# Performance work log

Measured on AMD Instinct MI355X. Metric: run time of the kernel, lower is better.

The kernel has to match this reference:

```python
import jax, jax.numpy as jnp
import numpy as np


def setup_inputs() -> dict:
    key = jax.random.key(0)
    ks = jax.random.split(key, 10)
    B, T, D = 256, 256, 256
    CH, L, K = 128, 3, 10          # chunk_size, levels, conv_size
    H = CH * L                     # hidden_dim = 384
    G = 4 * H + 2 * L              # gate projection width = 1542
    HS = H // 6

    def xavier(k, shape):
        fan_in, fan_out = shape[0], shape[-1]
        lim = np.sqrt(6.0 / (fan_in + fan_out)).astype(np.float32)
        return jax.random.uniform(k, shape, jnp.float32, -lim, lim)

    x = jax.random.normal(ks[0], (B, T, D), jnp.float32)
    lengths = jax.random.randint(ks[1], (B,), 1, T + 1).astype(jnp.int64)
    Wk = xavier(ks[2], (D + 1, G)); bk = jnp.zeros((G,), jnp.float32)
    Wr = xavier(ks[3], (H + 1, G)); br = jnp.zeros((G,), jnp.float32)
    Ws = xavier(ks[4], (H, HS));    bs = jnp.zeros((HS,), jnp.float32)
    Wrs = xavier(ks[5], (HS, H));   brs = jnp.zeros((H,), jnp.float32)
    Wc = xavier(ks[6], (H, H, K)) / np.sqrt(K)  # Conv1d weight (out, in, k)
    bc = jnp.zeros((H,), jnp.float32)
    return {"x": x, "lengths": lengths, "Wk": Wk, "bk": bk, "Wr": Wr,
            "br": br, "Ws": Ws, "bs": bs, "Wrs": Wrs, "brs": brs,
            "Wc": Wc, "bc": bc}


def _cumax_l2r(z):
    return jnp.cumsum(jax.nn.softmax(z, axis=-1), axis=-1)


def _cumax_r2l(z):
    zf = jnp.flip(z, -1)
    return jnp.flip(jnp.cumsum(jax.nn.softmax(zf, axis=-1), axis=-1), -1)


def reference(x, lengths, Wk, bk, Wr, br, Ws, bs, Wrs, brs, Wc, bc):
    B, T, D = x.shape
    H = Wr.shape[0] - 1
    G = Wk.shape[1]
    L = (G - 4 * H) // 2
    CH = H // L
    K = Wc.shape[2]
    ones = jnp.ones((B, 1), x.dtype)

    def step(carry, xt):
        c, h, tmp_h, tmp_dis = carry
        # two linear projections (interval == 1 always)
        xo = (jnp.concatenate([xt, ones], -1) @ Wk + bk
              + jnp.concatenate([h, ones], -1) @ Wr + br)
        fm = _cumax_l2r(xo[:, :L])[:, :, None]          # (B,L,1)
        im = _cumax_r2l(xo[:, L:2 * L])[:, :, None]     # (B,L,1)
        rest = xo[:, 2 * L:].reshape(B, 4 * L, CH)
        f = jax.nn.sigmoid(rest[:, :L])
        i = jax.nn.sigmoid(rest[:, L:2 * L])
        o = jax.nn.sigmoid(rest[:, 2 * L:3 * L])
        c_in = jnp.tanh(rest[:, 3 * L:])
        c_last = c.reshape(B, L, CH)
        ov = fm * im
        c_new = (ov * (f * c_last + i * c_in)
                 + (fm - ov) * c_last + (im - ov) * c_in)
        h_new = (o * jnp.tanh(c_new)).reshape(B, H)
        c_new = c_new.reshape(B, H)
        cur_dis = 1.0 - jnp.mean(fm[..., 0], axis=-1)   # (B,)
        # sliding buffers (K, B, H) and (K, B)
        tmp_h = jnp.concatenate([tmp_h[1:], h_new[None]], 0)
        tmp_dis = jnp.concatenate([tmp_dis[1:], cur_dis[None]], 0)
        # local window attention weights
        ld = jax.nn.softmax(jnp.cumsum(tmp_dis.T, axis=1), axis=1)  # (B,K)
        local_h = tmp_h.transpose(1, 2, 0) * ld[:, None, :]         # (B,H,K)
        theme = jax.nn.sigmoid(
            jax.nn.relu(jnp.mean(local_h, -1) @ Ws + bs) @ Wrs + brs)
        conv = jnp.einsum('bhk,ohk->bo', local_h, Wc) + bc          # valid conv -> len 1
        local_out = theme * conv
        return (c_new, h_new, tmp_h, tmp_dis), (h_new, local_out)

    c0 = jnp.zeros((B, H), x.dtype)
    h0 = jnp.zeros((B, H), x.dtype)
    th0 = jnp.zeros((K, B, H), x.dtype)
    td0 = jnp.zeros((K, B), x.dtype)
    _, (origin_h, loc_h) = jax.lax.scan(step, (c0, h0, th0, td0),
                                        x.transpose(1, 0, 2))
    output = (loc_h + origin_h).transpose(1, 0, 2)   # (B,T,H)
    idx = jnp.clip(lengths, 1, T).astype(jnp.int32) - 1
    last_output = output[jnp.arange(B), idx]
    return (last_output, output)
```

## Files before the change

### kernel.cpp

```cpp
#include <hip/hip_runtime.h>
#include <hip/hip_bf16.h>
#include <cstddef>

#define B_  256
#define T_  256
#define D_  256
#define H_  384
#define G_  1542
#define L_  3
#define CH_ 128
#define K_  10
#define HS_ 64

#define NGRP 16
#define NMEM 16
#define GW   16
#define CPM  24
#define NFR  7
#define PCOLS 112
#define XOLP 114
#define NKC  20
#define W_LDS    (NKC * NFR * 64 * 8 * 2)
#define BIAS_OFF W_LDS
#define UNI_OFF  (W_LDS + 512)
#define LDS_BYTES (UNI_OFF + 12288)

#define POST_LDS 107520

#define SENT 0xFFFFFFFFFFFFFFFFull

using bf16x8 = __attribute__((ext_vector_type(8))) short;
using f32x4  = __attribute__((ext_vector_type(4))) float;
typedef unsigned long long ull_t;

__device__ __forceinline__ float bf2f(unsigned short s) {
    return __uint_as_float(((unsigned)s) << 16);
}
__device__ __forceinline__ unsigned short f2bf(float f) {
    unsigned u = __float_as_uint(f);
    return (unsigned short)((u + 0x7fffu + ((u >> 16) & 1u)) >> 16);
}
__device__ __forceinline__ float sig_fast(float x) { return 1.f / (1.f + __expf(-x)); }
__device__ __forceinline__ float tanh_fast(float x) {
    float ax = fabsf(x);
    float t = __expf(-2.f * ax);
    float r = (1.f - t) / (1.f + t);
    return copysignf(r, x);
}
__device__ __forceinline__ ull_t ldA(const ull_t* p) {
    return __hip_atomic_load(p, __ATOMIC_RELAXED, __HIP_MEMORY_SCOPE_AGENT);
}
__device__ __forceinline__ bool rdy(ull_t v) {
    ull_t x = ~v;
    return (((x - 0x0001000100010001ull) & ~x & 0x8000800080008000ull) == 0ull);
}

__device__ __forceinline__ int gcol_of(int member, int p) {
    if (p < 6) return p;
    if (p < 102) { int q = p - 6; return 6 + (q / CPM) * H_ + member * CPM + (q % CPM); }
    return -1;
}

__global__ __launch_bounds__(256)
void k_xa(const float* __restrict__ x, unsigned short* __restrict__ xA) {
    __shared__ float xl[64][261];
    const int t = blockIdx.x, bq = blockIdx.y;
    const int b0 = bq * 64, tid = threadIdx.x;
    for (int idx = tid; idx < 4096; idx += 256) {
        int row = idx >> 6, c4 = idx & 63;
        float4 v = *(const float4*)(x + ((size_t)(b0 + row) * T_ + t) * D_ + c4 * 4);
        xl[row][c4 * 4 + 0] = v.x; xl[row][c4 * 4 + 1] = v.y;
        xl[row][c4 * 4 + 2] = v.z; xl[row][c4 * 4 + 3] = v.w;
    }
    __syncthreads();
    for (int idx = tid; idx < 2048; idx += 256) {
        int lane = idx & 63, gl = (idx >> 6) & 3, kc = idx >> 8;
        int brow = gl * 16 + (lane & 15);
        int d = kc * 32 + (lane >> 4) * 8;
        unsigned o[4];
        #pragma unroll
        for (int q = 0; q < 4; ++q)
            o[q] = (unsigned)f2bf(xl[brow][d + 2 * q])
                 | ((unsigned)f2bf(xl[brow][d + 2 * q + 1]) << 16);
        int4 pk = make_int4((int)o[0], (int)o[1], (int)o[2], (int)o[3]);
        ((int4*)xA)[(((size_t)t * 8 + kc) * 16 + (bq * 4 + gl)) * 64 + lane] = pk;
    }
}

__global__ __launch_bounds__(256)
void k_prep(const float* __restrict__ Wk, const float* __restrict__ bk,
            const float* __restrict__ Wr, const float* __restrict__ br,
            const float* __restrict__ Ws, const float* __restrict__ Wrs,
            const float* __restrict__ Wc,
            unsigned short* __restrict__ hbf, unsigned short* __restrict__ Wf,
            unsigned short* __restrict__ Wg, unsigned short* __restrict__ WsT,
            unsigned short* __restrict__ WrsT, float* __restrict__ biasP)
{
    const int bid = blockIdx.x, tid = threadIdx.x;
    if (bid < 2048) {
        ull_t* hb = (ull_t*)hbf;
        int base = bid * 256 + tid;
        #pragma unroll
        for (int j = 0; j < 12; ++j)
            __hip_atomic_store(hb + base + j * 524288, SENT,
                               __ATOMIC_RELAXED, __HIP_MEMORY_SCOPE_AGENT);
    } else if (bid < 2608) {
        int idx = (bid - 2048) * 256 + tid;
        int lane = idx & 63;
        int ni   = (idx >> 6) % NFR;
        int kc   = (idx / (64 * NFR)) % NKC;
        int member = idx / (64 * NFR * NKC);
        int p = ni * 16 + (lane & 15);
        int g = gcol_of(member, p);
        unsigned short out[8];
        #pragma unroll
        for (int j = 0; j < 8; ++j) {
            int k = kc * 32 + (lane >> 4) * 8 + j;
            float v = 0.f;
            if (g >= 0) v = (k < 256) ? Wk[(size_t)k * G_ + g] : Wr[(size_t)(k - 256) * G_ + g];
            out[j] = f2bf(v);
        }
        int4 pk;
        pk.x = (unsigned)out[0] | ((unsigned)out[1] << 16);
        pk.y = (unsigned)out[2] | ((unsigned)out[3] << 16);
        pk.z = (unsigned)out[4] | ((unsigned)out[5] << 16);
        pk.w = (unsigned)out[6] | ((unsigned)out[7] << 16);
        ((int4*)Wf)[idx] = pk;
    } else if (bid < 8368) {
        int idx = (bid - 2608) * 256 + tid;
        int o = idx / (K_ * H_);
        int rem = idx % (K_ * H_);
        int k = rem / H_, h = rem % H_;
        Wg[idx] = f2bf(Wc[((size_t)o * H_ + h) * K_ + k]);
    } else if (bid < 8464) {
        int idx = (bid - 8368) * 256 + tid;
        int jj = idx / H_, k = idx % H_;
        WsT[idx] = f2bf(Ws[(size_t)k * HS_ + jj]);
    } else if (bid < 8560) {
        int idx = (bid - 8464) * 256 + tid;
        int o = idx / HS_, jj = idx % HS_;
        WrsT[idx] = f2bf(Wrs[(size_t)jj * H_ + o]);
    } else {
        int idx = (bid - 8560) * 256 + tid;
        if (idx < NMEM * PCOLS) {
            int member = idx / PCOLS, p = idx % PCOLS;
            int g = gcol_of(member, p);
            biasP[idx] = (g >= 0)
                ? bk[g] + br[g] + Wk[(size_t)256 * G_ + g] + Wr[(size_t)384 * G_ + g] : 0.f;
        }
    }
}

__global__ __launch_bounds__(512, 1)
void k_serial(const unsigned short* __restrict__ xA, const unsigned short* __restrict__ Wf,
              const float* __restrict__ biasP,
              unsigned short* __restrict__ hbf, float* __restrict__ dis)
{
    extern __shared__ char lds_raw[];
    unsigned short* Wl = (unsigned short*)lds_raw;
    float* biasL = (float*)(lds_raw + BIAS_OFF);
    char* uni = lds_raw + UNI_OFF;
    float* xol = (float*)uni;
    int4* stage4 = (int4*)uni;
    const bf16x8* stage = (const bf16x8*)uni;

    const int tid = threadIdx.x;
    const int lane = tid & 63, wave = tid >> 6;
    const int group = blockIdx.x & 15, member = blockIdx.x >> 4;
    const int b0 = group * GW;
    const int ni = wave;
    const bool domm = (wave < NFR);

    {
        const int4* src = (const int4*)(Wf + (size_t)member * (NKC * NFR * 64 * 8));
        for (int i = tid; i < W_LDS / 16; i += 512) ((int4*)Wl)[i] = src[i];
        if (tid < PCOLS) biasL[tid] = biasP[member * PCOLS + tid];
    }
    __syncthreads();

    const float bias_a = domm ? biasL[ni * 16 + (lane & 15)] : 0.f;

    const bool hasS = (tid < 384);
    const int skcl = tid >> 6, sln = tid & 63;
    const int stA = skcl * 64 + sln;
    const int stB = (skcl + 6) * 64 + sln;
    const unsigned short* src0 =
        hbf + (size_t)(b0 + (sln & 15)) * H_ + skcl * 32 + (sln >> 4) * 8;

    float c_r0 = 0.f;

    for (int t = 0; t < T_; ++t) {
        bf16x8 xf[8];
        if (domm) {
            #pragma unroll
            for (int kc = 0; kc < 8; ++kc)
                xf[kc] = *((const bf16x8*)(xA
                    + (((size_t)t * 8 + kc) * 16 + group) * 512 + lane * 8));
        }

        f32x4 accA = f32x4{bias_a, bias_a, bias_a, bias_a};
        f32x4 accB = f32x4{0.f, 0.f, 0.f, 0.f};

        if (t > 0) {
            const size_t toff = (size_t)(t - 1) * B_ * H_;
            const ull_t* pA = (const ull_t*)(src0 + toff);
            const ull_t* pB = (const ull_t*)(src0 + toff + 192);
            ull_t v0 = SENT, v1 = SENT, v2 = SENT, v3 = SENT;
            if (hasS) { v0 = ldA(pA); v1 = ldA(pA + 1); v2 = ldA(pB); v3 = ldA(pB + 1); }

            if (domm) {
                #pragma unroll
                for (int kc = 0; kc < 8; ++kc) {
                    bf16x8 w0 = ((const bf16x8*)Wl)[(kc * NFR + ni) * 64 + lane];
                    if (kc & 1)
                        accB = __builtin_amdgcn_mfma_f32_16x16x32_bf16(xf[kc], w0, accB, 0, 0, 0);
                    else
                        accA = __builtin_amdgcn_mfma_f32_16x16x32_bf16(xf[kc], w0, accA, 0, 0, 0);
                }
            }

            if (hasS) {
                while (!(rdy(v0) && rdy(v1) && rdy(v2) && rdy(v3))) {
                    v0 = ldA(pA); v1 = ldA(pA + 1); v2 = ldA(pB); v3 = ldA(pB + 1);
                }
                stage4[stA] = make_int4((int)(v0 & 0xffffffffu), (int)(v0 >> 32),
                                        (int)(v1 & 0xffffffffu), (int)(v1 >> 32));
                stage4[stB] = make_int4((int)(v2 & 0xffffffffu), (int)(v2 >> 32),
                                        (int)(v3 & 0xffffffffu), (int)(v3 >> 32));
            }
            __syncthreads();
            if (domm) {
                #pragma unroll
                for (int kcl = 0; kcl < 12; ++kcl) {
                    bf16x8 a0 = stage[kcl * 64 + lane];
                    bf16x8 w0 = ((const bf16x8*)Wl)[((8 + kcl) * NFR + ni) * 64 + lane];
                    if (kcl & 1)
                        accB = __builtin_amdgcn_mfma_f32_16x16x32_bf16(a0, w0, accB, 0, 0, 0);
                    else
                        accA = __builtin_amdgcn_mfma_f32_16x16x32_bf16(a0, w0, accA, 0, 0, 0);
                }
            }
            __syncthreads();
        } else {
            if (domm) {
                #pragma unroll
                for (int kc = 0; kc < 8; ++kc) {
                    bf16x8 w0 = ((const bf16x8*)Wl)[(kc * NFR + ni) * 64 + lane];
                    if (kc & 1)
                        accB = __builtin_amdgcn_mfma_f32_16x16x32_bf16(xf[kc], w0, accB, 0, 0, 0);
                    else
                        accA = __builtin_amdgcn_mfma_f32_16x16x32_bf16(xf[kc], w0, accA, 0, 0, 0);
                }
            }
        }

        if (domm) {
            #pragma unroll
            for (int r = 0; r < 4; ++r)
                xol[((lane >> 4) * 4 + r) * XOLP + ni * 16 + (lane & 15)] = accA[r] + accB[r];
        }
        __syncthreads();

        if (tid < 384) {
            int b = tid & 15, ch = tid >> 4;
            const float* row = xol + b * XOLP;
            float z0 = row[0], z1 = row[1], z2 = row[2];
            float z3 = row[3], z4 = row[4], z5 = row[5];
            float m1 = fmaxf(fmaxf(z0, z1), z2);
            float e0 = __expf(z0 - m1), e1 = __expf(z1 - m1), e2 = __expf(z2 - m1);
            float inv1 = 1.f / (e0 + e1 + e2);
            float fm0 = e0 * inv1, fm1 = (e0 + e1) * inv1;
            float m2 = fmaxf(fmaxf(z3, z4), z5);
            float f3 = __expf(z3 - m2), f4 = __expf(z4 - m2), f5 = __expf(z5 - m2);
            float inv2 = 1.f / (f3 + f4 + f5);
            float im1 = (f4 + f5) * inv2, im2 = f5 * inv2;

            int hh = member * CPM + ch;
            int l = hh >> 7;
            float fm = (l == 0) ? fm0 : (l == 1) ? fm1 : 1.f;
            float im = (l == 0) ? 1.f : (l == 1) ? im1 : im2;

            float fg = sig_fast(row[6 + ch]);
            float ig = sig_fast(row[6 + CPM + ch]);
            float og = sig_fast(row[6 + 2 * CPM + ch]);
            float ci = tanh_fast(row[6 + 3 * CPM + ch]);

            float ov = fm * im;
            float cn = ov * (fg * c_r0 + ig * ci) + (fm - ov) * c_r0 + (im - ov) * ci;
            float hn = og * tanh_fast(cn);
            c_r0 = cn;

            unsigned hpk = (unsigned)f2bf(hn);
            unsigned partner = (unsigned)__shfl((int)hpk, (lane + 16) & 63);
            if (!(ch & 1)) {
                unsigned word = hpk | (partner << 16);
                __hip_atomic_store(
                    (unsigned*)(hbf + ((size_t)t * B_ + b0 + b) * H_ + hh),
                    word, __ATOMIC_RELAXED, __HIP_MEMORY_SCOPE_AGENT);
            }
            if (member == 0 && ch == 0)
                dis[t * B_ + b0 + b] = 1.f - (fm0 + fm1 + 1.f) * (1.f / 3.f);
        }
    }
}

__global__ __launch_bounds__(512, 1)
void k_post(const unsigned short* __restrict__ hbf, const float* __restrict__ dis,
            const unsigned short* __restrict__ Wg,
            const unsigned short* __restrict__ WsT, const unsigned short* __restrict__ WrsT,
            const float* __restrict__ bs, const float* __restrict__ brs,
            const float* __restrict__ bc, float* __restrict__ out_part)
{
    extern __shared__ char plds[];
    float* ldl = (float*)plds;
    unsigned short* AlB = (unsigned short*)(plds + 5120);
    unsigned short* BlB = (unsigned short*)(plds + 46080);
    unsigned short* hbarL = (unsigned short*)(plds + 5120);
    unsigned short* uL = (unsigned short*)(plds + 56320);

    const int bid = blockIdx.x + 4 * blockIdx.y;
    const int xcd = bid & 7, slot = bid >> 3;
    const int tpair = xcd * 16 + (slot >> 2);
    const int btile = slot & 3;
    const int b0 = btile * 64;
    const int t0 = tpair * 2;
    const int tid = threadIdx.x;
    const int wave = tid >> 6, lane = tid & 63;
    const int mh = wave >> 2, nq = wave & 3;

    if (tid < 128) {
        int ti = tid >> 6, bi = tid & 63;
        int t = t0 + ti, b = b0 + bi;
        float s = 0.f, sk[K_];
        #pragma unroll
        for (int k = 0; k < K_; ++k) {
            int tau = t - (K_ - 1) + k;
            float d = (tau >= 0) ? dis[tau * B_ + b] : 0.f;
            s += d; sk[k] = s;
        }
        float m = sk[0];
        #pragma unroll
        for (int k = 1; k < K_; ++k) m = fmaxf(m, sk[k]);
        float sum = 0.f;
        #pragma unroll
        for (int k = 0; k < K_; ++k) { sk[k] = __expf(sk[k] - m); sum += sk[k]; }
        float inv = 1.f / sum;
        #pragma unroll
        for (int k = 0; k < K_; ++k) ldl[ti * 640 + bi * 10 + k] = sk[k] * inv;
    }

    const int a_ti = tid >> 8, a_rem = tid & 255;
    const int a_bb = a_rem >> 2, a_half = a_rem & 3;

    auto loadA = [&](int ch, int4& av, bool& valid) {
        int k = ch / 12, hb = (ch % 12) * 32;
        int tau = t0 + a_ti - (K_ - 1) + k;
        valid = (tau >= 0);
        if (valid)
            av = *(const int4*)(hbf + ((size_t)tau * B_ + b0 + a_bb) * H_ + hb + a_half * 8);
    };
    auto loadB = [&](int ch, int4 bv[3]) {
        #pragma unroll
        for (int q = 0; q < 3; ++q) {
            int idx = q * 512 + tid;
            int row = idx >> 2, half = idx & 3;
            bv[q] = *(const int4*)(Wg + (size_t)row * 3840 + ch * 32 + half * 8);
        }
    };
    auto writeA = [&](int buf, int ch, int4 av, bool valid) {
        int k = ch / 12;
        int4 pk = make_int4(0, 0, 0, 0);
        if (valid) {
            float l = ldl[a_ti * 640 + a_bb * 10 + k];
            unsigned vv[4] = {(unsigned)av.x, (unsigned)av.y, (unsigned)av.z, (unsigned)av.w};
            unsigned o[4];
            #pragma unroll
            for (int q = 0; q < 4; ++q) {
                float flo = __uint_as_float(vv[q] << 16) * l;
                float fhi = __uint_as_float(vv[q] & 0xffff0000u) * l;
                o[q] = (unsigned)f2bf(flo) | ((unsigned)f2bf(fhi) << 16);
            }
            pk = make_int4((int)o[0], (int)o[1], (int)o[2], (int)o[3]);
        }
        *(int4*)&AlB[buf * 5120 + a_ti * 2560 + a_bb * 40 + a_half * 8] = pk;
    };
    auto writeB = [&](int buf, const int4 bv[3]) {
        #pragma unroll
        for (int q = 0; q < 3; ++q) {
            int idx = q * 512 + tid;
            int row = idx >> 2, half = idx & 3;
            *(int4*)&BlB[buf * 15360 + row * 40 + half * 8] = bv[q];
        }
    };

    int4 av; bool avalid; int4 bv[3];
    loadA(0, av, avalid); loadB(0, bv);
    __syncthreads();
    writeA(0, 0, av, avalid); writeB(0, bv);

    f32x4 acc[2][2][6] = {};
    for (int ch = 0; ch < 120; ++ch) {
        int cur = ch & 1;
        bool more = (ch + 1 < 120);
        if (more) { loadA(ch + 1, av, avalid); loadB(ch + 1, bv); }
        __syncthreads();
        if (more) { writeA(cur ^ 1, ch + 1, av, avalid); writeB(cur ^ 1, bv); }

        bf16x8 af[2][2];
        #pragma unroll
        for (int ti = 0; ti < 2; ++ti)
            #pragma unroll
            for (int mi = 0; mi < 2; ++mi)
                af[ti][mi] = *(const bf16x8*)&AlB[cur * 5120 + ti * 2560
                    + (mh * 32 + mi * 16 + (lane & 15)) * 40 + (lane >> 4) * 8];
        #pragma unroll
        for (int ni = 0; ni < 6; ++ni) {
            bf16x8 bfv = *(const bf16x8*)&BlB[cur * 15360
                + (nq * 96 + ni * 16 + (lane & 15)) * 40 + (lane >> 4) * 8];
            #pragma unroll
            for (int ti = 0; ti < 2; ++ti)
                #pragma unroll
                for (int mi = 0; mi < 2; ++mi)
                    acc[ti][mi][ni] = __builtin_amdgcn_mfma_f32_16x16x32_bf16(
                        af[ti][mi], bfv, acc[ti][mi][ni], 0, 0, 0);
        }
    }
    __syncthreads();

    #pragma unroll
    for (int ti = 0; ti < 2; ++ti) {
        const int t = t0 + ti;
        for (int idx = tid; idx < 3072; idx += 512) {
            int bb = idx / 48, h8 = idx % 48;
            float s[8] = {};
            #pragma unroll
            for (int k = 0; k < K_; ++k) {
                int tau = t - (K_ - 1) + k;
                if (tau >= 0) {
                    int4 v = *(const int4*)(hbf + ((size_t)tau * B_ + b0 + bb) * H_ + h8 * 8);
                    float l = ldl[ti * 640 + bb * 10 + k];
                    unsigned vv[4] = {(unsigned)v.x, (unsigned)v.y, (unsigned)v.z, (unsigned)v.w};
                    #pragma unroll
                    for (int q = 0; q < 4; ++q) {
                        s[2 * q]     = fmaf(__uint_as_float(vv[q] << 16), l, s[2 * q]);
                        s[2 * q + 1] = fmaf(__uint_as_float(vv[q] & 0xffff0000u), l, s[2 * q + 1]);
                    }
                }
            }
            unsigned o[4];
            #pragma unroll
            for (int q = 0; q < 4; ++q)
                o[q] = (unsigned)f2bf(s[2 * q] * 0.1f) | ((unsigned)f2bf(s[2 * q + 1] * 0.1f) << 16);
            *(int4*)&hbarL[bb * 400 + h8 * 8] = make_int4((int)o[0], (int)o[1], (int)o[2], (int)o[3]);
        }
        __syncthreads();

        if (wave < 4) {
            f32x4 uacc[4] = {};
            for (int kc = 0; kc < 12; ++kc) {
                bf16x8 a = *(const bf16x8*)&hbarL[(wave * 16 + (lane & 15)) * 400
                                                  + kc * 32 + (lane >> 4) * 8];
                #pragma unroll
                for (int ni = 0; ni < 4; ++ni) {
                    bf16x8 wb = *(const bf16x8*)(WsT + (size_t)(ni * 16 + (lane & 15)) * H_
                                                 + kc * 32 + (lane >> 4) * 8);
                    uacc[ni] = __builtin_amdgcn_mfma_f32_16x16x32_bf16(a, wb, uacc[ni], 0, 0, 0);
                }
            }
            #pragma unroll
            for (int ni = 0; ni < 4; ++ni) {
                float bsv = bs[ni * 16 + (lane & 15)];
                #pragma unroll
                for (int r = 0; r < 4; ++r)
                    uL[(wave * 16 + (lane >> 4) * 4 + r) * 72 + ni * 16 + (lane & 15)] =
                        f2bf(fmaxf(uacc[ni][r] + bsv, 0.f));
            }
        }
        __syncthreads();

        #pragma unroll
        for (int half = 0; half < 2; ++half) {
            f32x4 tacc[2][3] = {};
            #pragma unroll
            for (int kc = 0; kc < 2; ++kc) {
                bf16x8 ua[2];
                #pragma unroll
                for (int mi = 0; mi < 2; ++mi)
                    ua[mi] = *(const bf16x8*)&uL[(mh * 32 + mi * 16 + (lane & 15)) * 72
                                                 + kc * 32 + (lane >> 4) * 8];
                #pragma unroll
                for (int n3 = 0; n3 < 3; ++n3) {
                    int ni = half * 3 + n3;
                    bf16x8 wb = *(const bf16x8*)(WrsT
                        + (size_t)(nq * 96 + ni * 16 + (lane & 15)) * HS_
                        + kc * 32 + (lane >> 4) * 8);
                    #pragma unroll
                    for (int mi = 0; mi < 2; ++mi)
                        tacc[mi][n3] = __builtin_amdgcn_mfma_f32_16x16x32_bf16(
                            ua[mi], wb, tacc[mi][n3], 0, 0, 0);
                }
            }
            #pragma unroll
            for (int mi = 0; mi < 2; ++mi) {
                #pragma unroll
                for (int n3 = 0; n3 < 3; ++n3) {
                    int ni = half * 3 + n3;
                    int o = nq * 96 + ni * 16 + (lane & 15);
                    float brsv = brs[o], bcv = bc[o];
                    int brow0 = b0 + mh * 32 + mi * 16 + ((lane >> 4) << 2);
                    #pragma unroll
                    for (int r = 0; r < 4; ++r) {
                        float th = sig_fast(tacc[mi][n3][r] + brsv);
                        float cv = acc[ti][mi][ni][r] + bcv;
                        float hv = bf2f(hbf[((size_t)t * B_ + brow0 + r) * H_ + o]);
                        __builtin_nontemporal_store(hv + th * cv,
                            out_part + ((size_t)(brow0 + r) * T_ + t) * H_ + o);
                    }
                }
            }
        }
        __syncthreads();
    }
}

__global__ void k_last(const int* __restrict__ len_i, const float* __restrict__ out_part,
                       float* __restrict__ last)
{
    int b = blockIdx.x, tid = threadIdx.x;
    bool is64 = (len_i[1] == 0);
    long long v = is64 ? ((const long long*)len_i)[b] : (long long)len_i[b];
    int idx = (int)v;
    idx = max(1, min(T_, idx)) - 1;
    last[(size_t)b * H_ + tid] = out_part[((size_t)b * T_ + idx) * H_ + tid];
}

extern "C" void kernel_launch(void* const* d_in, const int* in_sizes, int n_in,
                              void* d_out, int out_size, void* d_ws, size_t ws_size,
                              hipStream_t stream) {
    const float* x   = (const float*)d_in[0];
    const int*   len = (const int*)d_in[1];
    const float* Wk  = (const float*)d_in[2];
    const float* bk  = (const float*)d_in[3];
    const float* Wr  = (const float*)d_in[4];
    const float* br  = (const float*)d_in[5];
    const float* Ws  = (const float*)d_in[6];
    const float* bs  = (const float*)d_in[7];
    const float* Wrs = (const float*)d_in[8];
    const float* brs = (const float*)d_in[9];
    const float* Wc  = (const float*)d_in[10];
    const float* bc  = (const float*)d_in[11];

    float* out      = (float*)d_out;
    float* last     = out;
    float* out_part = out + (size_t)B_ * H_;

    char* p = (char*)d_ws;
    float*          dis    = (float*)p;          p += (size_t)T_ * B_ * 4;
    unsigned short* xA     = (unsigned short*)p; p += (size_t)T_ * B_ * D_ * 2;
    unsigned short* WfragG = (unsigned short*)p; p += (size_t)NMEM * NKC * NFR * 64 * 8 * 2;
    float*          biasP  = (float*)p;          p += (size_t)NMEM * PCOLS * 4;
    unsigned short* hbf    = (unsigned short*)p; p += (size_t)T_ * B_ * H_ * 2;
    unsigned short* Wg     = (unsigned short*)p; p += (size_t)H_ * K_ * H_ * 2;
    unsigned short* WsT    = (unsigned short*)p; p += (size_t)HS_ * H_ * 2;
    unsigned short* WrsT   = (unsigned short*)p; p += (size_t)H_ * HS_ * 2;

    k_xa  <<<dim3(T_, 4), 256, 0, stream>>>(x, xA);
    k_prep<<<8567, 256, 0, stream>>>(Wk, bk, Wr, br, Ws, Wrs, Wc,
                                     hbf, WfragG, Wg, WsT, WrsT, biasP);

    hipFuncSetAttribute((const void*)k_serial,
                        hipFuncAttributeMaxDynamicSharedMemorySize, LDS_BYTES);
    hipFuncSetAttribute((const void*)k_post,
                        hipFuncAttributeMaxDynamicSharedMemorySize, POST_LDS);

    k_serial<<<NGRP * NMEM, 512, LDS_BYTES, stream>>>(xA, WfragG, biasP, hbf, dis);
    k_post <<<dim3(4, 128), 512, POST_LDS, stream>>>(hbf, dis, Wg, WsT, WrsT, bs, brs, bc, out_part);
    k_last <<<B_, H_, 0, stream>>>(len, out_part, last);
}
```

Measured before the change: 1.284 ms.

## Keep recurrent weight fragments in registers and separate staging from xol LDS

Each MFMA wave now loads its 20 weight fragments from global memory into registers once at kernel start, rather than copying the weights into LDS and reading them every timestep. The bias is read straight from global memory. The h staging buffer and the xol gate buffer now sit in separate LDS regions, which lets one __syncthreads per timestep be removed. The cost is about 80 extra VGPRs per thread, which could cause spills, and the correctness of removing the barrier depends on staging and xol no longer overlapping.

```diff
diff --git a/kernel.cpp b/kernel.cpp
--- a/kernel.cpp
+++ b/kernel.cpp
@@ -20,10 +20,9 @@
 #define PCOLS 112
 #define XOLP 114
 #define NKC  20
-#define W_LDS    (NKC * NFR * 64 * 8 * 2)
-#define BIAS_OFF W_LDS
-#define UNI_OFF  (W_LDS + 512)
-#define LDS_BYTES (UNI_OFF + 12288)
+#define STG_BYTES 12288
+#define XOL_OFF   STG_BYTES
+#define LDS_BYTES (STG_BYTES + XOLP * GW * 4)
 
 #define POST_LDS 107520
 
@@ -157,12 +156,9 @@
               unsigned short* __restrict__ hbf, float* __restrict__ dis)
 {
     extern __shared__ char lds_raw[];
-    unsigned short* Wl = (unsigned short*)lds_raw;
-    float* biasL = (float*)(lds_raw + BIAS_OFF);
-    char* uni = lds_raw + UNI_OFF;
-    float* xol = (float*)uni;
-    int4* stage4 = (int4*)uni;
-    const bf16x8* stage = (const bf16x8*)uni;
+    int4* stage4 = (int4*)lds_raw;
+    const bf16x8* stage = (const bf16x8*)lds_raw;
+    float* xol = (float*)(lds_raw + XOL_OFF);
 
     const int tid = threadIdx.x;
     const int lane = tid & 63, wave = tid >> 6;
@@ -171,14 +167,14 @@
     const int ni = wave;
     const bool domm = (wave < NFR);
 
-    {
-        const int4* src = (const int4*)(Wf + (size_t)member * (NKC * NFR * 64 * 8));
-        for (int i = tid; i < W_LDS / 16; i += 512) ((int4*)Wl)[i] = src[i];
-        if (tid < PCOLS) biasL[tid] = biasP[member * PCOLS + tid];
-    }
-    __syncthreads();
-
-    const float bias_a = domm ? biasL[ni * 16 + (lane & 15)] : 0.f;
+    bf16x8 wreg[NKC];
+    if (domm) {
+        const bf16x8* wsrc = (const bf16x8*)(Wf + (size_t)member * (NKC * NFR * 64 * 8));
+        #pragma unroll
+        for (int kc = 0; kc < NKC; ++kc)
+            wreg[kc] = wsrc[(kc * NFR + ni) * 64 + lane];
+    }
+    const float bias_a = domm ? biasP[member * PCOLS + ni * 16 + (lane & 15)] : 0.f;
 
     const bool hasS = (tid < 384);
     const int skcl = tid >> 6, sln = tid & 63;
@@ -211,11 +207,10 @@
             if (domm) {
                 #pragma unroll
                 for (int kc = 0; kc < 8; ++kc) {
-                    bf16x8 w0 = ((const bf16x8*)Wl)[(kc * NFR + ni) * 64 + lane];
                     if (kc & 1)
-                        accB = __builtin_amdgcn_mfma_f32_16x16x32_bf16(xf[kc], w0, accB, 0, 0, 0);
+                        accB = __builtin_amdgcn_mfma_f32_16x16x32_bf16(xf[kc], wreg[kc], accB, 0, 0, 0);
                     else
-                        accA = __builtin_amdgcn_mfma_f32_16x16x32_bf16(xf[kc], w0, accA, 0, 0, 0);
+                        accA = __builtin_amdgcn_mfma_f32_16x16x32_bf16(xf[kc], wreg[kc], accA, 0, 0, 0);
                 }
             }
 
@@ -233,23 +228,20 @@
                 #pragma unroll
                 for (int kcl = 0; kcl < 12; ++kcl) {
                     bf16x8 a0 = stage[kcl * 64 + lane];
-                    bf16x8 w0 = ((const bf16x8*)Wl)[((8 + kcl) * NFR + ni) * 64 + lane];
                     if (kcl & 1)
-                        accB = __builtin_amdgcn_mfma_f32_16x16x32_bf16(a0, w0, accB, 0, 0, 0);
+                        accB = __builtin_amdgcn_mfma_f32_16x16x32_bf16(a0, wreg[8 + kcl], accB, 0, 0, 0);
                     else
-                        accA = __builtin_amdgcn_mfma_f32_16x16x32_bf16(a0, w0, accA, 0, 0, 0);
-                }
-            }
-            __syncthreads();
+                        accA = __builtin_amdgcn_mfma_f32_16x16x32_bf16(a0, wreg[8 + kcl], accA, 0, 0, 0);
+                }
+            }
         } else {
             if (domm) {
                 #pragma unroll
                 for (int kc = 0; kc < 8; ++kc) {
-                    bf16x8 w0 = ((const bf16x8*)Wl)[(kc * NFR + ni) * 64 + lane];
                     if (kc & 1)
-                        accB = __builtin_amdgcn_mfma_f32_16x16x32_bf16(xf[kc], w0, accB, 0, 0, 0);
+                        accB = __builtin_amdgcn_mfma_f32_16x16x32_bf16(xf[kc], wreg[kc], accB, 0, 0, 0);
                     else
-                        accA = __builtin_amdgcn_mfma_f32_16x16x32_bf16(xf[kc], w0, accA, 0, 0, 0);
+                        accA = __builtin_amdgcn_mfma_f32_16x16x32_bf16(xf[kc], wreg[kc], accA, 0, 0, 0);
                 }
             }
         }
```

Result: faster. 1.245 ms, median of 2 (-3.0%).
